# Kernel tuning notes

Measured on AMD Instinct MI355X. Metric: run time of the kernel, lower is better.

Reference implementation:

```python
import jax, jax.numpy as jnp
import numpy as np

B, T_ENC, D_IN, H, T_OUT = 64, 49, 54, 1152, 25


def setup_inputs() -> dict:
    key = jax.random.key(0)
    ks = iter(jax.random.split(key, 40))
    u = lambda shape: jax.random.uniform(next(ks), shape, jnp.float32, -0.04, 0.04)
    n = lambda shape: 0.1 * jax.random.normal(next(ks), shape, jnp.float32)
    inp = {
        "hidden_states": n((B, T_ENC, H)),
        "cell_states": n((B, T_ENC, H)),
        "global_t_state": n((B, H)),
        "p": n((B, 1, D_IN)),
    }
    # four distinct LSTMCells: 0 (input), 1 (spine), A (shared by layers 2,3), L (shared by 4,5)
    for tag, din in [("0", D_IN), ("1", H), ("A", H), ("L", H)]:
        inp[f"Wih{tag}"] = u((4 * H, din))
        inp[f"Whh{tag}"] = u((4 * H, H))
        inp[f"bih{tag}"] = u((4 * H,))
        inp[f"bhh{tag}"] = u((4 * H,))
    for name, dim in [("spine", 12), ("leg1", 12), ("leg2", 12), ("arm1", 9), ("arm2", 9)]:
        inp[f"W_{name}"] = u((H, dim))
        inp[f"b_{name}"] = u((dim,))
    return inp


def _lstm_cell(x, h, c, Wih, Whh, bih, bhh):
    # PyTorch LSTMCell: gates ordered i, f, g, o
    g = x @ Wih.T + h @ Whh.T + bih + bhh
    i, f, gg, o = jnp.split(g, 4, axis=-1)
    c2 = jax.nn.sigmoid(f) * c + jax.nn.sigmoid(i) * jnp.tanh(gg)
    h2 = jax.nn.sigmoid(o) * jnp.tanh(c2)
    return h2, c2


def reference(hidden_states, cell_states, global_t_state, p,
              Wih0, Whh0, bih0, bhh0, Wih1, Whh1, bih1, bhh1,
              WihA, WhhA, bihA, bhhA, WihL, WhhL, bihL, bhhL,
              W_spine, b_spine, W_leg1, b_leg1, W_leg2, b_leg2,
              W_arm1, b_arm1, W_arm2, b_arm2):
    b = hidden_states.shape[0]
    hd = hidden_states.shape[-1]
    c_init = cell_states.mean(axis=1)
    h0 = hidden_states.mean(axis=1)
    h1 = jnp.concatenate([global_t_state[:, None, :], hidden_states], axis=1).mean(axis=1)
    z = jnp.zeros((b, hd), hidden_states.dtype)
    carry0 = (p[:, 0, :], h0, c_init, h1, c_init, z, z, z, z, z, z, z, z)

    def step(carry, _):
        x0, h0, c0, h1, c1, h2, c2, h3, c3, h4, c4, h5, c5 = carry
        h0n, c0n = _lstm_cell(x0, h0, c0, Wih0, Whh0, bih0, bhh0)
        h1n, c1n = _lstm_cell(h0n, h1, c1, Wih1, Whh1, bih1, bhh1)
        h2n, c2n = _lstm_cell(h1n, h2, c2, WihA, WhhA, bihA, bhhA)
        # source bug: `i == (3 or 4 or 5)` is `i == 3`, so layer 3 reads h[1],
        # layers 4,5 fall through to h[i-1]
        h3n, c3n = _lstm_cell(h1n, h3, c3, WihA, WhhA, bihA, bhhA)
        h4n, c4n = _lstm_cell(h3n, h4, c4, WihL, WhhL, bihL, bhhL)
        h5n, c5n = _lstm_cell(h4n, h5, c5, WihL, WhhL, bihL, bhhL)
        # residual output heads; index sets are contiguous column blocks of pre
        leg1 = h2n @ W_leg1 + b_leg1 + x0[:, 0:12]
        leg2 = h3n @ W_leg2 + b_leg2 + x0[:, 12:24]
        spine = h1n @ W_spine + b_spine + x0[:, 24:36]
        arm1 = h4n @ W_arm1 + b_arm1 + x0[:, 36:45]
        arm2 = h5n @ W_arm2 + b_arm2 + x0[:, 45:54]
        pre = jnp.concatenate([leg1, leg2, spine, arm1, arm2], axis=-1)
        new_carry = (pre, h0n, c0n, h1n, c1n, h2n, c2n, h3n, c3n, h4n, c4n, h5n, c5n)
        return new_carry, pre

    _, pres = jax.lax.scan(step, carry0, None, length=T_OUT)  # [T, B, D_IN]
    return jnp.transpose(pres, (1, 0, 2))  # [B, T, D_IN]
```

## Files before the change

### kernel.cpp

```cpp
#include <hip/hip_runtime.h>
#include <math.h>

typedef unsigned short u16;
typedef short s16x8 __attribute__((ext_vector_type(8)));
typedef float f32x4 __attribute__((ext_vector_type(4)));

#define DEV __device__ __forceinline__

constexpr int B = 64, H = 1152, G4 = 4608, TOUT = 25, TENC = 49;
constexpr int NKH = 36;

constexpr size_t SZW       = (size_t)G4 * H;
constexpr size_t OFF_W     = 0;
constexpr size_t OFF_WIH0P = OFF_W + 7 * SZW * 2;
constexpr size_t OFF_WHT   = OFF_WIH0P + (size_t)G4 * 64 * 2;
constexpr size_t OFF_BIAS  = OFF_WHT + (size_t)5 * 16 * H * 2;
constexpr size_t OFF_H     = OFF_BIAS + (size_t)4 * G4 * 4;
constexpr size_t HBUF      = (size_t)6 * B * H * 2;
constexpr size_t OFF_C     = OFF_H + 2 * HBUF;
constexpr size_t OFF_GH    = OFF_C + (size_t)6 * B * H * 4;
constexpr size_t OFF_X0    = OFF_GH + (size_t)5 * B * G4 * 4;
constexpr size_t OFF_X0B   = OFF_X0 + (size_t)B * 64 * 4;

DEV u16 f2bf(float f){ union { float f; unsigned u; } v; v.f = f;
  unsigned r = v.u + 0x7fffu + ((v.u >> 16) & 1u); return (u16)(r >> 16); }
DEV f32x4 mfma16(s16x8 a, s16x8 b, f32x4 c){ return __builtin_amdgcn_mfma_f32_16x16x32_bf16(a, b, c, 0, 0, 0); }
DEV s16x8 ld8(const u16* p){ return *reinterpret_cast<const s16x8*>(p); }
DEV float sigf(float x){ return 1.0f / (1.0f + expf(-x)); }

DEV u16*   WBF(char* ws, int i){ return (u16*)(ws + OFF_W) + (size_t)i * SZW; }
DEV u16*   HPK(char* ws, int buf, int cell){ return (u16*)(ws + OFF_H + (size_t)buf * HBUF) + (size_t)cell * B * H; }
DEV float* CPK(char* ws, int cell){ return (float*)(ws + OFF_C) + (size_t)cell * B * H; }
DEV float* GHK(char* ws, int c1){ return (float*)(ws + OFF_GH) + (size_t)c1 * B * G4; }

struct PrepW {
  const float* big[7];
  const float* wih0;
  const float* wh[5];
  const float* bih[4];
  const float* bhh[4];
};

__global__ __launch_bounds__(256) void k_prepw(char* ws, PrepW pa){
  const int r = blockIdx.y;
  const size_t tid = (size_t)blockIdx.x * 256 + threadIdx.x;
  const size_t stride = (size_t)gridDim.x * 256;
  if(r < 7){
    unsigned* dst = (unsigned*)WBF(ws, r);
    const float* src = pa.big[r];
    const size_t n2 = SZW / 2;
    for(size_t i = tid; i < n2; i += stride){
      float a = src[2*i], b = src[2*i+1];
      dst[i] = (unsigned)f2bf(a) | ((unsigned)f2bf(b) << 16);
    }
  } else if(r == 7){
    u16* dst = (u16*)(ws + OFF_WIH0P);
    for(size_t i = tid; i < (size_t)G4 * 64; i += stride){
      int row = (int)(i >> 6), k = (int)(i & 63);
      dst[i] = (k < 54) ? f2bf(pa.wih0[(size_t)row * 54 + k]) : (u16)0;
    }
  } else if(r == 8){
    const int HD[5] = {12,12,12,9,9};
    u16* dst = (u16*)(ws + OFF_WHT);
    for(size_t i = tid; i < (size_t)5 * 16 * H; i += stride){
      int h = (int)(i / (16 * H));
      int rem = (int)(i - (size_t)h * 16 * H);
      int n = rem / H, k = rem % H;
      dst[i] = (n < HD[h]) ? f2bf(pa.wh[h][(size_t)k * HD[h] + n]) : (u16)0;
    }
  } else {
    float* dst = (float*)(ws + OFF_BIAS);
    for(size_t i = tid; i < (size_t)4 * G4; i += stride){
      int tag = (int)(i / G4), j = (int)(i % G4);
      dst[i] = pa.bih[tag][j] + pa.bhh[tag][j];
    }
  }
}

__global__ __launch_bounds__(256) void k_preps(char* ws, const float* hs, const float* cs,
                                               const float* gts, const float* p){
  int idx = blockIdx.x * 256 + threadIdx.x;
  if(idx >= B * H) return;
  int b = idx / H, k = idx % H;
  float sh = 0.f, sc = 0.f;
  for(int t = 0; t < TENC; ++t){
    sh += hs[((size_t)b * TENC + t) * H + k];
    sc += cs[((size_t)b * TENC + t) * H + k];
  }
  float h0 = sh * (1.0f / 49.0f);
  float h1 = (gts[(size_t)b * H + k] + sh) * (1.0f / 50.0f);
  float ci = sc * (1.0f / 49.0f);
  HPK(ws,0,0)[idx] = f2bf(h0);
  HPK(ws,0,1)[idx] = f2bf(h1);
  HPK(ws,0,2)[idx] = 0; HPK(ws,0,3)[idx] = 0; HPK(ws,0,4)[idx] = 0; HPK(ws,0,5)[idx] = 0;
  CPK(ws,0)[idx] = ci; CPK(ws,1)[idx] = ci;
  CPK(ws,2)[idx] = 0.f; CPK(ws,3)[idx] = 0.f; CPK(ws,4)[idx] = 0.f; CPK(ws,5)[idx] = 0.f;
  if(k < 64){
    ((u16*)(ws + OFF_X0B))[b * 64 + k] = (k < 54) ? f2bf(p[(size_t)b * 54 + k]) : (u16)0;
    if(k < 54) ((float*)(ws + OFF_X0))[b * 64 + k] = p[(size_t)b * 54 + k];
  }
}

__global__ __launch_bounds__(64) void k_ph1(char* ws, int rp){
  const int lane = threadIdx.x, l15 = lane & 15, lk = lane >> 4;
  const int bid = blockIdx.x;
  const int cell = bid / 72;
  const int jb = (bid % 72) * 16;
  const int widx_c[6] = {0,2,4,4,6,6};
  const int btag_c[6] = {0,1,2,2,3,3};
  const u16* W = WBF(ws, widx_c[cell]);
  const u16* A = HPK(ws, rp, cell);

  f32x4 acc[4][4] = {};
  #pragma unroll 2
  for(int kk = 0; kk < NKH; ++kk){
    const int ko = kk * 32 + lk * 8;
    s16x8 a[4], b[4];
    #pragma unroll
    for(int mt = 0; mt < 4; ++mt) a[mt] = ld8(A + (size_t)(mt*16 + l15) * H + ko);
    #pragma unroll
    for(int g = 0; g < 4; ++g)   b[g]  = ld8(W + (size_t)(g*H + jb + l15) * H + ko);
    #pragma unroll
    for(int mt = 0; mt < 4; ++mt)
      #pragma unroll
      for(int g = 0; g < 4; ++g) acc[mt][g] = mfma16(a[mt], b[g], acc[mt][g]);
  }

  if(cell == 0){
    const u16* Wx = (const u16*)(ws + OFF_WIH0P);
    const u16* X  = (const u16*)(ws + OFF_X0B);
    #pragma unroll
    for(int kk = 0; kk < 2; ++kk){
      const int ko = kk * 32 + lk * 8;
      s16x8 a[4], b[4];
      #pragma unroll
      for(int mt = 0; mt < 4; ++mt) a[mt] = ld8(X + (size_t)(mt*16 + l15) * 64 + ko);
      #pragma unroll
      for(int g = 0; g < 4; ++g)   b[g]  = ld8(Wx + (size_t)(g*H + jb + l15) * 64 + ko);
      #pragma unroll
      for(int mt = 0; mt < 4; ++mt)
        #pragma unroll
        for(int g = 0; g < 4; ++g) acc[mt][g] = mfma16(a[mt], b[g], acc[mt][g]);
    }
    const float* bias = (const float*)(ws + OFF_BIAS);
    float* Cc = CPK(ws, 0);
    u16*   Hn = HPK(ws, rp ^ 1, 0);
    #pragma unroll
    for(int mt = 0; mt < 4; ++mt)
      #pragma unroll
      for(int r = 0; r < 4; ++r){
        int row = mt*16 + lk*4 + r, col = jb + l15;
        float gi = acc[mt][0][r] + bias[col];
        float gf = acc[mt][1][r] + bias[H + col];
        float gg = acc[mt][2][r] + bias[2*H + col];
        float go = acc[mt][3][r] + bias[3*H + col];
        float co = Cc[(size_t)row*H + col];
        float cn = sigf(gf)*co + sigf(gi)*tanhf(gg);
        Cc[(size_t)row*H + col] = cn;
        Hn[(size_t)row*H + col] = f2bf(sigf(go)*tanhf(cn));
      }
  } else {
    const float* bias = (const float*)(ws + OFF_BIAS) + (size_t)btag_c[cell] * G4;
    float* gh = GHK(ws, cell - 1);
    #pragma unroll
    for(int mt = 0; mt < 4; ++mt)
      #pragma unroll
      for(int g = 0; g < 4; ++g)
        #pragma unroll
        for(int r = 0; r < 4; ++r){
          int row = mt*16 + lk*4 + r, col = jb + l15;
          gh[(size_t)row*G4 + g*H + col] = acc[mt][g][r] + bias[g*H + col];
        }
  }
}

__global__ __launch_bounds__(64) void k_cellx(char* ws, int rp, int cell, int src, int widx){
  const int lane = threadIdx.x, l15 = lane & 15, lk = lane >> 4;
  const int bid = blockIdx.x;
  const int mt = bid & 3;
  const int jb = (bid >> 2) * 16;
  const u16* W = WBF(ws, widx);
  const u16* A = HPK(ws, rp ^ 1, src);

  f32x4 acc[4] = {};
  #pragma unroll 2
  for(int kk = 0; kk < NKH; ++kk){
    const int ko = kk * 32 + lk * 8;
    s16x8 a = ld8(A + (size_t)(mt*16 + l15) * H + ko);
    #pragma unroll
    for(int g = 0; g < 4; ++g){
      s16x8 b = ld8(W + (size_t)(g*H + jb + l15) * H + ko);
      acc[g] = mfma16(a, b, acc[g]);
    }
  }
  const float* gh = GHK(ws, cell - 1);
  float* Cc = CPK(ws, cell);
  u16*   Hn = HPK(ws, rp ^ 1, cell);
  #pragma unroll
  for(int r = 0; r < 4; ++r){
    int row = mt*16 + lk*4 + r, col = jb + l15;
    const float* ghr = gh + (size_t)row*G4 + col;
    float gi = acc[0][r] + ghr[0];
    float gf = acc[1][r] + ghr[H];
    float gg = acc[2][r] + ghr[2*H];
    float go = acc[3][r] + ghr[3*H];
    float co = Cc[(size_t)row*H + col];
    float cn = sigf(gf)*co + sigf(gi)*tanhf(gg);
    Cc[(size_t)row*H + col] = cn;
    Hn[(size_t)row*H + col] = f2bf(sigf(go)*tanhf(cn));
  }
}

__global__ __launch_bounds__(64) void k_pair(char* ws, int rp){
  const int lane = threadIdx.x, l15 = lane & 15, lk = lane >> 4;
  const int bid = blockIdx.x;
  const int mt = bid & 3;
  const int jb = (bid >> 2) * 16;
  const u16* W = WBF(ws, 3);
  const u16* A = HPK(ws, rp ^ 1, 1);

  f32x4 acc[4] = {};
  #pragma unroll 2
  for(int kk = 0; kk < NKH; ++kk){
    const int ko = kk * 32 + lk * 8;
    s16x8 a = ld8(A + (size_t)(mt*16 + l15) * H + ko);
    #pragma unroll
    for(int g = 0; g < 4; ++g){
      s16x8 b = ld8(W + (size_t)(g*H + jb + l15) * H + ko);
      acc[g] = mfma16(a, b, acc[g]);
    }
  }
  #pragma unroll
  for(int cell = 2; cell <= 3; ++cell){
    const float* gh = GHK(ws, cell - 1);
    float* Cc = CPK(ws, cell);
    u16*   Hn = HPK(ws, rp ^ 1, cell);
    #pragma unroll
    for(int r = 0; r < 4; ++r){
      int row = mt*16 + lk*4 + r, col = jb + l15;
      const float* ghr = gh + (size_t)row*G4 + col;
      float gi = acc[0][r] + ghr[0];
      float gf = acc[1][r] + ghr[H];
      float gg = acc[2][r] + ghr[2*H];
      float go = acc[3][r] + ghr[3*H];
      float co = Cc[(size_t)row*H + col];
      float cn = sigf(gf)*co + sigf(gi)*tanhf(gg);
      Cc[(size_t)row*H + col] = cn;
      Hn[(size_t)row*H + col] = f2bf(sigf(go)*tanhf(cn));
    }
  }
}

__global__ __launch_bounds__(256) void k_heads(char* ws, int rp, float* out, int t,
    const float* bh0, const float* bh1, const float* bh2, const float* bh3, const float* bh4){
  const int head = blockIdx.x;
  const int w = threadIdx.x >> 6;
  const int lane = threadIdx.x & 63, l15 = lane & 15, lk = lane >> 4;
  const int HD[5] = {12,12,12,9,9}, HOFF[5] = {0,12,24,36,45}, HSRC[5] = {2,3,1,4,5};
  const u16* A  = HPK(ws, rp ^ 1, HSRC[head]);
  const u16* Wt = (const u16*)(ws + OFF_WHT) + (size_t)head * 16 * H;
  const float* bh = head==0?bh0 : head==1?bh1 : head==2?bh2 : head==3?bh3 : bh4;

  f32x4 acc = {};
  #pragma unroll 2
  for(int kk = 0; kk < NKH; ++kk){
    const int ko = kk * 32 + lk * 8;
    s16x8 a = ld8(A + (size_t)(w*16 + l15) * H + ko);
    s16x8 b = ld8(Wt + (size_t)l15 * H + ko);
    acc = mfma16(a, b, acc);
  }
  float* x0  = (float*)(ws + OFF_X0);
  u16*   x0b = (u16*)(ws + OFF_X0B);
  const int n = l15;
  if(n < HD[head]){
    #pragma unroll
    for(int r = 0; r < 4; ++r){
      int row = w*16 + lk*4 + r;
      int c = HOFF[head] + n;
      float val = acc[r] + bh[n] + x0[row*64 + c];
      out[((size_t)row*TOUT + t)*54 + c] = val;
      x0[row*64 + c] = val;
      x0b[row*64 + c] = f2bf(val);
    }
  }
}

extern "C" void kernel_launch(void* const* d_in, const int* in_sizes, int n_in,
                              void* d_out, int out_size, void* d_ws, size_t ws_size,
                              hipStream_t stream){
  (void)in_sizes; (void)n_in; (void)out_size; (void)ws_size;
  char* ws = (char*)d_ws;
  float* out = (float*)d_out;
  const float* hs  = (const float*)d_in[0];
  const float* cs  = (const float*)d_in[1];
  const float* gts = (const float*)d_in[2];
  const float* p   = (const float*)d_in[3];

  PrepW pa;
  pa.big[0] = (const float*)d_in[5];
  pa.big[1] = (const float*)d_in[8];
  pa.big[2] = (const float*)d_in[9];
  pa.big[3] = (const float*)d_in[12];
  pa.big[4] = (const float*)d_in[13];
  pa.big[5] = (const float*)d_in[16];
  pa.big[6] = (const float*)d_in[17];
  pa.wih0   = (const float*)d_in[4];
  pa.wh[0]  = (const float*)d_in[22];
  pa.wh[1]  = (const float*)d_in[24];
  pa.wh[2]  = (const float*)d_in[20];
  pa.wh[3]  = (const float*)d_in[26];
  pa.wh[4]  = (const float*)d_in[28];
  pa.bih[0] = (const float*)d_in[6];  pa.bhh[0] = (const float*)d_in[7];
  pa.bih[1] = (const float*)d_in[10]; pa.bhh[1] = (const float*)d_in[11];
  pa.bih[2] = (const float*)d_in[14]; pa.bhh[2] = (const float*)d_in[15];
  pa.bih[3] = (const float*)d_in[18]; pa.bhh[3] = (const float*)d_in[19];

  hipLaunchKernelGGL(k_prepw, dim3(2048, 10), dim3(256), 0, stream, ws, pa);
  hipLaunchKernelGGL(k_preps, dim3(288), dim3(256), 0, stream, ws, hs, cs, gts, p);

  for(int t = 0; t < TOUT; ++t){
    const int rp = t & 1;
    hipLaunchKernelGGL(k_ph1,   dim3(432), dim3(64), 0, stream, ws, rp);
    hipLaunchKernelGGL(k_cellx, dim3(288), dim3(64), 0, stream, ws, rp, 1, 0, 1);
    hipLaunchKernelGGL(k_pair,  dim3(288), dim3(64), 0, stream, ws, rp);
    hipLaunchKernelGGL(k_cellx, dim3(288), dim3(64), 0, stream, ws, rp, 4, 3, 5);
    hipLaunchKernelGGL(k_cellx, dim3(288), dim3(64), 0, stream, ws, rp, 5, 4, 5);
    hipLaunchKernelGGL(k_heads, dim3(5), dim3(256), 0, stream, ws, rp, out, t,
        (const float*)d_in[23], (const float*)d_in[25], (const float*)d_in[21],
        (const float*)d_in[27], (const float*)d_in[29]);
  }
}
```

Before: 2.892 ms.

## Replace per-step kernel launches with persistent kernel using grid barriers

Replaces the 150 per-timestep kernel launches with a single persistent kernel of 72 blocks × 512 threads that loops over all timesteps and syncs between layer phases with a global atomic barrier. Each block owns a 16-column slice and splits the K reduction across 8 waves, combining partial sums through shared memory. The precomputed gate buffer is gone because input and recurrent GEMMs now run inside the same phase, and the weight conversion is vectorised to float4 loads. Only 72 blocks run on a large GPU, each streaming all weights per step, and the spin barrier relies on every block being co-resident.

```diff
diff --git a/kernel.cpp b/kernel.cpp
--- a/kernel.cpp
+++ b/kernel.cpp
@@ -3,12 +3,13 @@
 
 typedef unsigned short u16;
 typedef short s16x8 __attribute__((ext_vector_type(8)));
+typedef u16 u16x4 __attribute__((ext_vector_type(4)));
 typedef float f32x4 __attribute__((ext_vector_type(4)));
 
 #define DEV __device__ __forceinline__
 
 constexpr int B = 64, H = 1152, G4 = 4608, TOUT = 25, TENC = 49;
-constexpr int NKH = 36;
+constexpr unsigned NBLK = 72;
 
 constexpr size_t SZW       = (size_t)G4 * H;
 constexpr size_t OFF_W     = 0;
@@ -18,9 +19,9 @@
 constexpr size_t OFF_H     = OFF_BIAS + (size_t)4 * G4 * 4;
 constexpr size_t HBUF      = (size_t)6 * B * H * 2;
 constexpr size_t OFF_C     = OFF_H + 2 * HBUF;
-constexpr size_t OFF_GH    = OFF_C + (size_t)6 * B * H * 4;
-constexpr size_t OFF_X0    = OFF_GH + (size_t)5 * B * G4 * 4;
+constexpr size_t OFF_X0    = OFF_C + (size_t)6 * B * H * 4;
 constexpr size_t OFF_X0B   = OFF_X0 + (size_t)B * 64 * 4;
+constexpr size_t OFF_BAR   = OFF_X0B + (size_t)B * 64 * 2;
 
 DEV u16 f2bf(float f){ union { float f; unsigned u; } v; v.f = f;
   unsigned r = v.u + 0x7fffu + ((v.u >> 16) & 1u); return (u16)(r >> 16); }
@@ -31,7 +32,24 @@
 DEV u16*   WBF(char* ws, int i){ return (u16*)(ws + OFF_W) + (size_t)i * SZW; }
 DEV u16*   HPK(char* ws, int buf, int cell){ return (u16*)(ws + OFF_H + (size_t)buf * HBUF) + (size_t)cell * B * H; }
 DEV float* CPK(char* ws, int cell){ return (float*)(ws + OFF_C) + (size_t)cell * B * H; }
-DEV float* GHK(char* ws, int c1){ return (float*)(ws + OFF_GH) + (size_t)c1 * B * G4; }
+
+DEV void gridbar(unsigned* bar){
+  __syncthreads();
+  if(threadIdx.x == 0){
+    __threadfence();
+    unsigned g = __hip_atomic_load(bar + 1, __ATOMIC_RELAXED, __HIP_MEMORY_SCOPE_AGENT);
+    unsigned a = __hip_atomic_fetch_add(bar, 1u, __ATOMIC_RELAXED, __HIP_MEMORY_SCOPE_AGENT);
+    if(a == NBLK - 1u){
+      __hip_atomic_store(bar, 0u, __ATOMIC_RELAXED, __HIP_MEMORY_SCOPE_AGENT);
+      __hip_atomic_store(bar + 1, g + 1u, __ATOMIC_RELEASE, __HIP_MEMORY_SCOPE_AGENT);
+    } else {
+      while(__hip_atomic_load(bar + 1, __ATOMIC_RELAXED, __HIP_MEMORY_SCOPE_AGENT) == g)
+        __builtin_amdgcn_s_sleep(1);
+    }
+    __threadfence();
+  }
+  __syncthreads();
+}
 
 struct PrepW {
   const float* big[7];
@@ -46,12 +64,13 @@
   const size_t tid = (size_t)blockIdx.x * 256 + threadIdx.x;
   const size_t stride = (size_t)gridDim.x * 256;
   if(r < 7){
-    unsigned* dst = (unsigned*)WBF(ws, r);
-    const float* src = pa.big[r];
-    const size_t n2 = SZW / 2;
-    for(size_t i = tid; i < n2; i += stride){
-      float a = src[2*i], b = src[2*i+1];
-      dst[i] = (unsigned)f2bf(a) | ((unsigned)f2bf(b) << 16);
+    const float4* src = (const float4*)pa.big[r];
+    u16x4* dst = (u16x4*)WBF(ws, r);
+    const size_t n4 = SZW / 4;
+    for(size_t i = tid; i < n4; i += stride){
+      float4 v = src[i];
+      u16x4 o = { f2bf(v.x), f2bf(v.y), f2bf(v.z), f2bf(v.w) };
+      dst[i] = o;
     }
   } else if(r == 7){
     u16* dst = (u16*)(ws + OFF_WIH0P);
@@ -81,6 +100,10 @@
                                                const float* gts, const float* p){
   int idx = blockIdx.x * 256 + threadIdx.x;
   if(idx >= B * H) return;
+  if(idx == 0){
+    unsigned* bar = (unsigned*)(ws + OFF_BAR);
+    bar[0] = 0u; bar[1] = 0u;
+  }
   int b = idx / H, k = idx % H;
   float sh = 0.f, sc = 0.f;
   for(int t = 0; t < TENC; ++t){
@@ -101,187 +124,158 @@
   }
 }
 
-__global__ __launch_bounds__(64) void k_ph1(char* ws, int rp){
-  const int lane = threadIdx.x, l15 = lane & 15, lk = lane >> 4;
-  const int bid = blockIdx.x;
-  const int cell = bid / 72;
-  const int jb = (bid % 72) * 16;
-  const int widx_c[6] = {0,2,4,4,6,6};
-  const int btag_c[6] = {0,1,2,2,3,3};
-  const u16* W = WBF(ws, widx_c[cell]);
-  const u16* A = HPK(ws, rp, cell);
-
-  f32x4 acc[4][4] = {};
-  #pragma unroll 2
-  for(int kk = 0; kk < NKH; ++kk){
-    const int ko = kk * 32 + lk * 8;
-    s16x8 a[4], b[4];
+
+DEV void accum_range(f32x4* acc, const u16* A, int ldA, const u16* W, int ldW,
+                     int mt, int jb, int l15, int lk, int c0, int c1){
+  const u16* ar = A + (size_t)(mt*16 + l15) * ldA + lk*8;
+  const u16* wr = W + (size_t)(jb + l15) * ldW + lk*8;
+  #pragma unroll 3
+  for(int kk = c0; kk < c1; ++kk){
+    s16x8 a = ld8(ar + (size_t)kk*32);
     #pragma unroll
-    for(int mt = 0; mt < 4; ++mt) a[mt] = ld8(A + (size_t)(mt*16 + l15) * H + ko);
+    for(int g = 0; g < 4; ++g)
+      acc[g] = mfma16(a, ld8(wr + (size_t)g*H*ldW + (size_t)kk*32), acc[g]);
+  }
+}
+
+DEV void reduce_epi(float* red, const f32x4* acc, int w, int lane, int l15, int lk,
+                    int jb, const float* bias, float* Cc, u16* Hn){
+  __syncthreads();
+  if(w >= 4){
+    const int mt = w - 4;
     #pragma unroll
-    for(int g = 0; g < 4; ++g)   b[g]  = ld8(W + (size_t)(g*H + jb + l15) * H + ko);
+    for(int g = 0; g < 4; ++g)
+      *reinterpret_cast<f32x4*>(&red[((mt*4+g)*64 + lane)*4]) = acc[g];
+  }
+  __syncthreads();
+  if(w < 4){
+    const int mt = w;
+    const int col = jb + l15;
     #pragma unroll
-    for(int mt = 0; mt < 4; ++mt)
-      #pragma unroll
-      for(int g = 0; g < 4; ++g) acc[mt][g] = mfma16(a[mt], b[g], acc[mt][g]);
-  }
-
-  if(cell == 0){
-    const u16* Wx = (const u16*)(ws + OFF_WIH0P);
-    const u16* X  = (const u16*)(ws + OFF_X0B);
-    #pragma unroll
-    for(int kk = 0; kk < 2; ++kk){
-      const int ko = kk * 32 + lk * 8;
-      s16x8 a[4], b[4];
-      #pragma unroll
-      for(int mt = 0; mt < 4; ++mt) a[mt] = ld8(X + (size_t)(mt*16 + l15) * 64 + ko);
-      #pragma unroll
-      for(int g = 0; g < 4; ++g)   b[g]  = ld8(Wx + (size_t)(g*H + jb + l15) * 64 + ko);
-      #pragma unroll
-      for(int mt = 0; mt < 4; ++mt)
-        #pragma unroll
-        for(int g = 0; g < 4; ++g) acc[mt][g] = mfma16(a[mt], b[g], acc[mt][g]);
-    }
-    const float* bias = (const float*)(ws + OFF_BIAS);
-    float* Cc = CPK(ws, 0);
-    u16*   Hn = HPK(ws, rp ^ 1, 0);
-    #pragma unroll
-    for(int mt = 0; mt < 4; ++mt)
-      #pragma unroll
-      for(int r = 0; r < 4; ++r){
-        int row = mt*16 + lk*4 + r, col = jb + l15;
-        float gi = acc[mt][0][r] + bias[col];
-        float gf = acc[mt][1][r] + bias[H + col];
-        float gg = acc[mt][2][r] + bias[2*H + col];
-        float go = acc[mt][3][r] + bias[3*H + col];
-        float co = Cc[(size_t)row*H + col];
-        float cn = sigf(gf)*co + sigf(gi)*tanhf(gg);
-        Cc[(size_t)row*H + col] = cn;
-        Hn[(size_t)row*H + col] = f2bf(sigf(go)*tanhf(cn));
-      }
-  } else {
-    const float* bias = (const float*)(ws + OFF_BIAS) + (size_t)btag_c[cell] * G4;
-    float* gh = GHK(ws, cell - 1);
-    #pragma unroll
-    for(int mt = 0; mt < 4; ++mt)
+    for(int r = 0; r < 4; ++r){
+      const int row = mt*16 + lk*4 + r;
+      float G[4];
       #pragma unroll
       for(int g = 0; g < 4; ++g)
+        G[g] = acc[g][r] + red[((mt*4+g)*64 + lane)*4 + r] + bias[(size_t)g*H + col];
+      float co = Cc[(size_t)row*H + col];
+      float cn = sigf(G[1])*co + sigf(G[0])*tanhf(G[2]);
+      Cc[(size_t)row*H + col] = cn;
+      Hn[(size_t)row*H + col] = f2bf(sigf(G[3])*tanhf(cn));
+    }
+  }
+}
+
+DEV void cell_phase(float* red, int w, int lane, int l15, int lk, int jb,
+                    const u16* Ain, const u16* Wih, const u16* Aself, const u16* Whh,
+                    const float* bias, float* Cc, u16* Hn){
+  const int mt = w & 3;
+  f32x4 acc[4] = {};
+  if(w < 4) accum_range(acc, Ain,   H, Wih, H, mt, jb, l15, lk, 0, 36);
+  else      accum_range(acc, Aself, H, Whh, H, mt, jb, l15, lk, 0, 36);
+  reduce_epi(red, acc, w, lane, l15, lk, jb, bias, Cc, Hn);
+}
+
+__global__ __launch_bounds__(512, 1) void k_persist(char* ws, float* out,
+    const float* bh0, const float* bh1, const float* bh2, const float* bh3, const float* bh4)
+{
+  const int w = threadIdx.x >> 6;
+  const int lane = threadIdx.x & 63;
+  const int l15 = lane & 15, lk = lane >> 4;
+  const int bid = blockIdx.x;
+  const int jb = bid * 16;
+  const int mt = w & 3;
+
+  __shared__ float red[16 * 64 * 4];
+  unsigned* bar = (unsigned*)(ws + OFF_BAR);
+
+  const float* bias = (const float*)(ws + OFF_BIAS);
+  float* x0  = (float*)(ws + OFF_X0);
+  u16*   x0b = (u16*)(ws + OFF_X0B);
+  const u16* Wx = (const u16*)(ws + OFF_WIH0P);
+
+  for(int t = 0; t < TOUT; ++t){
+    const int rp = t & 1;
+
+    {
+      f32x4 acc[4] = {};
+      if(w < 4){
+        accum_range(acc, x0b, 64, Wx, 64, mt, jb, l15, lk, 0, 2);
+        accum_range(acc, HPK(ws,rp,0), H, WBF(ws,0), H, mt, jb, l15, lk, 0, 17);
+      } else {
+        accum_range(acc, HPK(ws,rp,0), H, WBF(ws,0), H, mt, jb, l15, lk, 17, 36);
+      }
+      reduce_epi(red, acc, w, lane, l15, lk, jb, bias, CPK(ws,0), HPK(ws,rp^1,0));
+    }
+    gridbar(bar);
+
+    cell_phase(red, w, lane, l15, lk, jb,
+               HPK(ws,rp^1,0), WBF(ws,1), HPK(ws,rp,1), WBF(ws,2),
+               bias + G4, CPK(ws,1), HPK(ws,rp^1,1));
+    gridbar(bar);
+
+    {
+      const u16* A1 = HPK(ws, rp^1, 1);
+      const u16* WihA = WBF(ws,3);
+      const u16* WhhA = WBF(ws,4);
+      const float* b2 = bias + 2*(size_t)G4;
+      f32x4 accA[4] = {};
+      if(w < 4) accum_range(accA, A1, H, WihA, H, mt, jb, l15, lk, 0, 36);
+      else      accum_range(accA, HPK(ws,rp,2), H, WhhA, H, mt, jb, l15, lk, 0, 36);
+      reduce_epi(red, accA, w, lane, l15, lk, jb, b2, CPK(ws,2), HPK(ws,rp^1,2));
+      f32x4 acc3[4];
+      if(w < 4){
+        #pragma unroll
+        for(int g = 0; g < 4; ++g) acc3[g] = accA[g];
+        accum_range(acc3, HPK(ws,rp,3), H, WhhA, H, mt, jb, l15, lk, 18, 36);
+      } else {
+        #pragma unroll
+        for(int g = 0; g < 4; ++g) acc3[g] = (f32x4){0.f,0.f,0.f,0.f};
+        accum_range(acc3, HPK(ws,rp,3), H, WhhA, H, mt, jb, l15, lk, 0, 18);
+      }
+      reduce_epi(red, acc3, w, lane, l15, lk, jb, b2, CPK(ws,3), HPK(ws,rp^1,3));
+    }
+    gridbar(bar);
+
+    cell_phase(red, w, lane, l15, lk, jb,
+               HPK(ws,rp^1,3), WBF(ws,5), HPK(ws,rp,4), WBF(ws,6),
+               bias + 3*(size_t)G4, CPK(ws,4), HPK(ws,rp^1,4));
+    gridbar(bar);
+
+    cell_phase(red, w, lane, l15, lk, jb,
+               HPK(ws,rp^1,4), WBF(ws,5), HPK(ws,rp,5), WBF(ws,6),
+               bias + 3*(size_t)G4, CPK(ws,5), HPK(ws,rp^1,5));
+    gridbar(bar);
+
+    if(bid < 5){
+      const int HD[5] = {12,12,12,9,9}, HOFF[5] = {0,12,24,36,45}, HSRC[5] = {2,3,1,4,5};
+      const u16* A  = HPK(ws, rp^1, HSRC[bid]);
+      const u16* Wt = (const u16*)(ws + OFF_WHT) + (size_t)bid * 16 * H;
+      const float* bh = bid==0?bh0 : bid==1?bh1 : bid==2?bh2 : bid==3?bh3 : bh4;
+      const int half = w >> 2;
+      f32x4 acc = {};
+      const u16* ar = A + (size_t)(mt*16 + l15) * H + half*576 + lk*8;
+      const u16* wr = Wt + (size_t)l15 * H + half*576 + lk*8;
+      #pragma unroll 3
+      for(int kk = 0; kk < 18; ++kk)
+        acc = mfma16(ld8(ar + kk*32), ld8(wr + kk*32), acc);
+      __syncthreads();
+      if(w >= 4)
+        *reinterpret_cast<f32x4*>(&red[((w-4)*64 + lane)*4]) = acc;
+      __syncthreads();
+      if(w < 4 && l15 < HD[bid]){
         #pragma unroll
         for(int r = 0; r < 4; ++r){
-          int row = mt*16 + lk*4 + r, col = jb + l15;
-          gh[(size_t)row*G4 + g*H + col] = acc[mt][g][r] + bias[g*H + col];
+          const int row = mt*16 + lk*4 + r;
+          const int c = HOFF[bid] + l15;
+          float val = acc[r] + red[(mt*64 + lane)*4 + r] + bh[l15] + x0[row*64 + c];
+          out[((size_t)row*TOUT + t)*54 + c] = val;
+          x0[row*64 + c] = val;
+          x0b[row*64 + c] = f2bf(val);
         }
-  }
-}
-
-__global__ __launch_bounds__(64) void k_cellx(char* ws, int rp, int cell, int src, int widx){
-  const int lane = threadIdx.x, l15 = lane & 15, lk = lane >> 4;
-  const int bid = blockIdx.x;
-  const int mt = bid & 3;
-  const int jb = (bid >> 2) * 16;
-  const u16* W = WBF(ws, widx);
-  const u16* A = HPK(ws, rp ^ 1, src);
-
-  f32x4 acc[4] = {};
-  #pragma unroll 2
-  for(int kk = 0; kk < NKH; ++kk){
-    const int ko = kk * 32 + lk * 8;
-    s16x8 a = ld8(A + (size_t)(mt*16 + l15) * H + ko);
-    #pragma unroll
-    for(int g = 0; g < 4; ++g){
-      s16x8 b = ld8(W + (size_t)(g*H + jb + l15) * H + ko);
-      acc[g] = mfma16(a, b, acc[g]);
-    }
-  }
-  const float* gh = GHK(ws, cell - 1);
-  float* Cc = CPK(ws, cell);
-  u16*   Hn = HPK(ws, rp ^ 1, cell);
-  #pragma unroll
-  for(int r = 0; r < 4; ++r){
-    int row = mt*16 + lk*4 + r, col = jb + l15;
-    const float* ghr = gh + (size_t)row*G4 + col;
-    float gi = acc[0][r] + ghr[0];
-    float gf = acc[1][r] + ghr[H];
-    float gg = acc[2][r] + ghr[2*H];
-    float go = acc[3][r] + ghr[3*H];
-    float co = Cc[(size_t)row*H + col];
-    float cn = sigf(gf)*co + sigf(gi)*tanhf(gg);
-    Cc[(size_t)row*H + col] = cn;
-    Hn[(size_t)row*H + col] = f2bf(sigf(go)*tanhf(cn));
-  }
-}
-
-__global__ __launch_bounds__(64) void k_pair(char* ws, int rp){
-  const int lane = threadIdx.x, l15 = lane & 15, lk = lane >> 4;
-  const int bid = blockIdx.x;
-  const int mt = bid & 3;
-  const int jb = (bid >> 2) * 16;
-  const u16* W = WBF(ws, 3);
-  const u16* A = HPK(ws, rp ^ 1, 1);
-
-  f32x4 acc[4] = {};
-  #pragma unroll 2
-  for(int kk = 0; kk < NKH; ++kk){
-    const int ko = kk * 32 + lk * 8;
-    s16x8 a = ld8(A + (size_t)(mt*16 + l15) * H + ko);
-    #pragma unroll
-    for(int g = 0; g < 4; ++g){
-      s16x8 b = ld8(W + (size_t)(g*H + jb + l15) * H + ko);
-      acc[g] = mfma16(a, b, acc[g]);
-    }
-  }
-  #pragma unroll
-  for(int cell = 2; cell <= 3; ++cell){
-    const float* gh = GHK(ws, cell - 1);
-    float* Cc = CPK(ws, cell);
-    u16*   Hn = HPK(ws, rp ^ 1, cell);
-    #pragma unroll
-    for(int r = 0; r < 4; ++r){
-      int row = mt*16 + lk*4 + r, col = jb + l15;
-      const float* ghr = gh + (size_t)row*G4 + col;
-      float gi = acc[0][r] + ghr[0];
-      float gf = acc[1][r] + ghr[H];
-      float gg = acc[2][r] + ghr[2*H];
-      float go = acc[3][r] + ghr[3*H];
-      float co = Cc[(size_t)row*H + col];
-      float cn = sigf(gf)*co + sigf(gi)*tanhf(gg);
-      Cc[(size_t)row*H + col] = cn;
-      Hn[(size_t)row*H + col] = f2bf(sigf(go)*tanhf(cn));
-    }
-  }
-}
-
-__global__ __launch_bounds__(256) void k_heads(char* ws, int rp, float* out, int t,
-    const float* bh0, const float* bh1, const float* bh2, const float* bh3, const float* bh4){
-  const int head = blockIdx.x;
-  const int w = threadIdx.x >> 6;
-  const int lane = threadIdx.x & 63, l15 = lane & 15, lk = lane >> 4;
-  const int HD[5] = {12,12,12,9,9}, HOFF[5] = {0,12,24,36,45}, HSRC[5] = {2,3,1,4,5};
-  const u16* A  = HPK(ws, rp ^ 1, HSRC[head]);
-  const u16* Wt = (const u16*)(ws + OFF_WHT) + (size_t)head * 16 * H;
-  const float* bh = head==0?bh0 : head==1?bh1 : head==2?bh2 : head==3?bh3 : bh4;
-
-  f32x4 acc = {};
-  #pragma unroll 2
-  for(int kk = 0; kk < NKH; ++kk){
-    const int ko = kk * 32 + lk * 8;
-    s16x8 a = ld8(A + (size_t)(w*16 + l15) * H + ko);
-    s16x8 b = ld8(Wt + (size_t)l15 * H + ko);
-    acc = mfma16(a, b, acc);
-  }
-  float* x0  = (float*)(ws + OFF_X0);
-  u16*   x0b = (u16*)(ws + OFF_X0B);
-  const int n = l15;
-  if(n < HD[head]){
-    #pragma unroll
-    for(int r = 0; r < 4; ++r){
-      int row = w*16 + lk*4 + r;
-      int c = HOFF[head] + n;
-      float val = acc[r] + bh[n] + x0[row*64 + c];
-      out[((size_t)row*TOUT + t)*54 + c] = val;
-      x0[row*64 + c] = val;
-      x0b[row*64 + c] = f2bf(val);
-    }
+      }
+    }
+    gridbar(bar);
   }
 }
 
@@ -318,15 +312,7 @@
   hipLaunchKernelGGL(k_prepw, dim3(2048, 10), dim3(256), 0, stream, ws, pa);
   hipLaunchKernelGGL(k_preps, dim3(288), dim3(256), 0, stream, ws, hs, cs, gts, p);
 
-  for(int t = 0; t < TOUT; ++t){
-    const int rp = t & 1;
-    hipLaunchKernelGGL(k_ph1,   dim3(432), dim3(64), 0, stream, ws, rp);
-    hipLaunchKernelGGL(k_cellx, dim3(288), dim3(64), 0, stream, ws, rp, 1, 0, 1);
-    hipLaunchKernelGGL(k_pair,  dim3(288), dim3(64), 0, stream, ws, rp);
-    hipLaunchKernelGGL(k_cellx, dim3(288), dim3(64), 0, stream, ws, rp, 4, 3, 5);
-    hipLaunchKernelGGL(k_cellx, dim3(288), dim3(64), 0, stream, ws, rp, 5, 4, 5);
-    hipLaunchKernelGGL(k_heads, dim3(5), dim3(256), 0, stream, ws, rp, out, t,
-        (const float*)d_in[23], (const float*)d_in[25], (const float*)d_in[21],
-        (const float*)d_in[27], (const float*)d_in[29]);
-  }
-}
+  hipLaunchKernelGGL(k_persist, dim3(NBLK), dim3(512), 0, stream, ws, out,
+                     (const float*)d_in[23], (const float*)d_in[25], (const float*)d_in[21],
+                     (const float*)d_in[27], (const float*)d_in[29]);
+}
```

After: 7.327 ms. 2.53x slower.
